# Performance work log

Measured on AMD Instinct MI355X. Metric: run time of the kernel, lower is better.

## Reference

```python
import jax, jax.numpy as jnp
import numpy as np

L_MAX = 5      # o3_lambda from 0..5 -> m sizes 1,3,5,7,9,11
N = 10000      # number of atomic environments (samples)
NF = 64        # number of radial/species features per block


def setup_inputs() -> dict:
    key = jax.random.key(0)
    inp = {}
    for l in range(L_MAX + 1):
        key, k = jax.random.split(key)
        inp[f"c{l}"] = jax.random.normal(k, (N, 2 * l + 1, NF), dtype=jnp.float32)
    return inp


def reference(c0, c1, c2, c3, c4, c5):
    # Per l: ps_l = (2l+1)^{-1/2} * sum_m c[n,m,f] * c[n,m,g]  -> (n, nf, nf)
    # i.e. a batched c^T @ c GEMM per sample, then flatten and concat over l.
    cs = [c0, c1, c2, c3, c4, c5]
    outs = []
    for l, c in enumerate(cs):
        cg = (2 * l + 1) ** (-0.5)
        ps = cg * jnp.einsum('nmf,nmg->nfg', c, c)  # (n, nf, nf)
        outs.append(ps.reshape(c.shape[0], -1))      # (n, nf*nf)
    return jnp.concatenate(outs, axis=-1)            # (n, (l_max+1)*nf^2)
```

## Files before the change

kernel.cpp:

```cpp
#include <hip/hip_runtime.h>


#define NF 64
#define NL 6

typedef float f4 __attribute__((ext_vector_type(4)));

__constant__ float CG[NL] = {
    1.0f,
    0.57735026918962576f,
    0.44721359549995794f,
    0.37796447300922722f,
    0.33333333333333333f,
    0.30151134457776363f
};

__global__ __launch_bounds__(256, 2) void ps_kernel(
    const float* __restrict__ c0, const float* __restrict__ c1,
    const float* __restrict__ c2, const float* __restrict__ c3,
    const float* __restrict__ c4, const float* __restrict__ c5,
    float* __restrict__ out)
{
    __shared__ float lds[2304];

    const float* cs[NL] = {c0, c1, c2, c3, c4, c5};
    const int n = blockIdx.x;
    const int tid = threadIdx.x;

#pragma unroll
    for (int l = 0; l < NL; ++l) {
        const int nm = 2 * l + 1;
        const f4* src = (const f4*)(cs[l] + (size_t)n * (nm * NF));
        f4* dst = (f4*)(lds + l * l * NF);
        const int cnt4 = nm * (NF / 4);
        for (int i = tid; i < cnt4; i += 256)
            dst[i] = __builtin_nontemporal_load(&src[i]);
    }
    __syncthreads();

    const int f0 = ((tid >> 4) << 2);
    const int g4 = ((tid & 15) << 2);

    float* outn = out + (size_t)n * (NL * NF * NF);

#pragma unroll
    for (int l = 0; l < NL; ++l) {
        const int nm = 2 * l + 1;
        const float* cl = lds + l * l * NF;
        const float cg = CG[l];

        f4 acc[4];
#pragma unroll
        for (int r = 0; r < 4; ++r) acc[r] = (f4)(0.f);

        for (int m = 0; m < nm; ++m) {
            const float* row = cl + m * NF;
            const f4 a = *(const f4*)(row + f0);
            const f4 b = *(const f4*)(row + g4);
#pragma unroll
            for (int r = 0; r < 4; ++r) {
                acc[r] += a[r] * b;
            }
        }

        float* po = outn + l * (NF * NF);
#pragma unroll
        for (int r = 0; r < 4; ++r) {
            f4 v = acc[r] * cg;
            __builtin_nontemporal_store(v, (f4*)(po + (size_t)(f0 + r) * NF + g4));
        }
    }
}

extern "C" void kernel_launch(void* const* d_in, const int* in_sizes, int n_in,
                              void* d_out, int out_size, void* d_ws, size_t ws_size,
                              hipStream_t stream) {
    const float* c0 = (const float*)d_in[0];
    const float* c1 = (const float*)d_in[1];
    const float* c2 = (const float*)d_in[2];
    const float* c3 = (const float*)d_in[3];
    const float* c4 = (const float*)d_in[4];
    const float* c5 = (const float*)d_in[5];
    float* outp = (float*)d_out;

    const int N = in_sizes[0] / NF;

    hipLaunchKernelGGL(ps_kernel, dim3(N), dim3(256), 0, stream,
                       c0, c1, c2, c3, c4, c5, outp);
}
```

Baseline: 1.031 ms.

## Use persistent grid with register-prefetched next sample and regular stores

Replaces the one-block-per-sample launch with a fixed grid of 2048 persistent blocks that loop over samples. Each block prefetches the next sample's inputs into registers while it computes and stores the current one, and load addresses are precomputed per thread. Nontemporal output stores become ordinary stores and occupancy hints are raised. The aim is to hide load latency and cut block launch overhead in this store-bound kernel, at the cost of an extra barrier per iteration and a possible change in write caching behaviour.

```diff
diff --git a/kernel.cpp b/kernel.cpp
--- a/kernel.cpp
+++ b/kernel.cpp
@@ -3,6 +3,7 @@
 
 #define NF 64
 #define NL 6
+#define GRID 2048
 
 typedef float f4 __attribute__((ext_vector_type(4)));
 
@@ -15,34 +16,8 @@
     0.30151134457776363f
 };
 
-__global__ __launch_bounds__(256, 2) void ps_kernel(
-    const float* __restrict__ c0, const float* __restrict__ c1,
-    const float* __restrict__ c2, const float* __restrict__ c3,
-    const float* __restrict__ c4, const float* __restrict__ c5,
-    float* __restrict__ out)
-{
-    __shared__ float lds[2304];
-
-    const float* cs[NL] = {c0, c1, c2, c3, c4, c5};
-    const int n = blockIdx.x;
-    const int tid = threadIdx.x;
-
-#pragma unroll
-    for (int l = 0; l < NL; ++l) {
-        const int nm = 2 * l + 1;
-        const f4* src = (const f4*)(cs[l] + (size_t)n * (nm * NF));
-        f4* dst = (f4*)(lds + l * l * NF);
-        const int cnt4 = nm * (NF / 4);
-        for (int i = tid; i < cnt4; i += 256)
-            dst[i] = __builtin_nontemporal_load(&src[i]);
-    }
-    __syncthreads();
-
-    const int f0 = ((tid >> 4) << 2);
-    const int g4 = ((tid & 15) << 2);
-
-    float* outn = out + (size_t)n * (NL * NF * NF);
-
+__device__ __forceinline__ void compute_store(const float* lds, int f0, int g4,
+                                              float* outn) {
 #pragma unroll
     for (int l = 0; l < NL; ++l) {
         const int nm = 2 * l + 1;
@@ -58,17 +33,67 @@
             const f4 a = *(const f4*)(row + f0);
             const f4 b = *(const f4*)(row + g4);
 #pragma unroll
-            for (int r = 0; r < 4; ++r) {
-                acc[r] += a[r] * b;
-            }
+            for (int r = 0; r < 4; ++r) acc[r] += a[r] * b;
         }
 
         float* po = outn + l * (NF * NF);
 #pragma unroll
         for (int r = 0; r < 4; ++r) {
             f4 v = acc[r] * cg;
-            __builtin_nontemporal_store(v, (f4*)(po + (size_t)(f0 + r) * NF + g4));
+            *(f4*)(po + (size_t)(f0 + r) * NF + g4) = v;
         }
+    }
+}
+
+__global__ __launch_bounds__(256, 8) void ps_final(
+    const float* __restrict__ c0, const float* __restrict__ c1,
+    const float* __restrict__ c2, const float* __restrict__ c3,
+    const float* __restrict__ c4, const float* __restrict__ c5,
+    float* __restrict__ out, int N)
+{
+    __shared__ float lds[2304];
+    const float* cs[NL] = {c0, c1, c2, c3, c4, c5};
+    const int tid = threadIdx.x;
+
+    const bool k2 = (tid < 64);
+    const f4* srcb[3];
+    int sstr[3];
+    f4* ldsp[3];
+#pragma unroll
+    for (int k = 0; k < 3; ++k) {
+        const int i = k * 256 + tid;
+        const int ic = (i < 576) ? i : 575;
+        int l = 0;
+        while ((l + 1) * (l + 1) * 16 <= ic) ++l;
+        const int off = ic - l * l * 16;
+        srcb[k] = (const f4*)cs[l] + off;
+        sstr[k] = (2 * l + 1) * 16;
+        ldsp[k] = (f4*)lds + ic;
+    }
+
+    const int f0 = ((tid >> 4) << 2);
+    const int g4 = ((tid & 15) << 2);
+
+    int n = blockIdx.x;
+    if (n >= N) return;
+
+    f4 r0 = srcb[0][(size_t)n * sstr[0]];
+    f4 r1 = srcb[1][(size_t)n * sstr[1]];
+    f4 r2 = k2 ? srcb[2][(size_t)n * sstr[2]] : (f4)(0.f);
+
+    for (; n < N; n += GRID) {
+        __syncthreads();
+        *ldsp[0] = r0;
+        *ldsp[1] = r1;
+        if (k2) *ldsp[2] = r2;
+        const int np = n + GRID;
+        if (np < N) {
+            r0 = srcb[0][(size_t)np * sstr[0]];
+            r1 = srcb[1][(size_t)np * sstr[1]];
+            if (k2) r2 = srcb[2][(size_t)np * sstr[2]];
+        }
+        __syncthreads();
+        compute_store(lds, f0, g4, out + (size_t)n * (NL * NF * NF));
     }
 }
 
@@ -85,6 +110,6 @@
 
     const int N = in_sizes[0] / NF;
 
-    hipLaunchKernelGGL(ps_kernel, dim3(N), dim3(256), 0, stream,
-                       c0, c1, c2, c3, c4, c5, outp);
+    hipLaunchKernelGGL(ps_final, dim3(GRID), dim3(256), 0, stream,
+                       c0, c1, c2, c3, c4, c5, outp, N);
 }
```

Result: no change. 1.026 ms (-0.5%).
